# Optimization experiments

Measured on AMD Instinct MI355X. Metric: run time of the kernel, lower is better.

The kernel has to match this reference:

```python
import jax, jax.numpy as jnp
import numpy as np

EPS = 1e-5
NEG_SLOPE = 0.1  # GeoTransformer UnaryBlock uses LeakyReLU(0.1)
GROUPS = 32


def linear(x, W, b):
    # torch nn.Linear convention: W is (out, in)
    return x @ W.T + b


def group_norm(x, gamma, beta, groups=GROUPS):
    # x: (N, C). Torch applies GroupNorm on (1, C, N): stats over (C//g * N) per group.
    N, C = x.shape
    xg = x.T.reshape(groups, -1)            # (g, C//g * N)
    m = xg.mean(axis=1, keepdims=True)
    v = xg.var(axis=1, keepdims=True)
    xn = ((xg - m) / jnp.sqrt(v + EPS)).reshape(C, N).T
    return xn * gamma + beta


def unary_block(x, W, b, gamma, beta):
    return jax.nn.leaky_relu(group_norm(linear(x, W, b), gamma, beta), NEG_SLOPE)


def setup_inputs() -> dict:
    key = jax.random.key(0)
    ks = jax.random.split(key, 24)
    init_dim = 64
    N2, N3, N4, N5 = 131072, 32768, 8192, 2048
    d2, d3, d4, d5 = init_dim * 4, init_dim * 8, init_dim * 16, 2048
    out_dim = 256
    s = lambda k, shp: jax.random.normal(k, shp, dtype=jnp.float32)
    inp = {
        'feats_s2': s(ks[0], (N2, d2)),
        'feats_s3': s(ks[1], (N3, d3)),
        'feats_s4': s(ks[2], (N4, d4)),
        'feats_s5': s(ks[3], (N5, d5)),
        'up1': jax.random.randint(ks[4], (N2,), 0, N3),
        'up2': jax.random.randint(ks[5], (N3,), 0, N4),
        'up3': jax.random.randint(ks[6], (N4,), 0, N5),
        # inproj: Linear(input_dim, init_dim*32)
        'W_in': s(ks[7], (init_dim * 32, d5)) * 0.02,
        'b_in': s(ks[8], (init_dim * 32,)) * 0.02,
        # decoder4: UnaryBlock(init_dim*48, init_dim*16)
        'W4': s(ks[9], (init_dim * 16, init_dim * 48)) * 0.02,
        'b4': s(ks[10], (init_dim * 16,)) * 0.02,
        'g4': jnp.ones((init_dim * 16,), jnp.float32),
        'beta4': jnp.zeros((init_dim * 16,), jnp.float32),
        # decoder3: UnaryBlock(init_dim*24, init_dim*8)
        'W3': s(ks[11], (init_dim * 8, init_dim * 24)) * 0.02,
        'b3': s(ks[12], (init_dim * 8,)) * 0.02,
        'g3': jnp.ones((init_dim * 8,), jnp.float32),
        'beta3': jnp.zeros((init_dim * 8,), jnp.float32),
        # decoder2: LastUnaryBlock(init_dim*12, output_dim) -> plain Linear
        'W2': s(ks[13], (out_dim, init_dim * 12)) * 0.02,
        'b2': s(ks[14], (out_dim,)) * 0.02,
    }
    return inp


def reference(feats_s2, feats_s3, feats_s4, feats_s5, up1, up2, up3,
              W_in, b_in, W4, b4, g4, beta4, W3, b3, g3, beta3, W2, b2):
    x5 = linear(feats_s5, W_in, b_in)                     # (N5, 2048)
    l4 = jnp.concatenate([x5[up3], feats_s4], axis=1)     # gather + concat (N4, 3072)
    l4 = unary_block(l4, W4, b4, g4, beta4)               # (N4, 1024)
    l3 = jnp.concatenate([l4[up2], feats_s3], axis=1)     # (N3, 1536)
    l3 = unary_block(l3, W3, b3, g3, beta3)               # (N3, 512)
    l2 = jnp.concatenate([l3[up1], feats_s2], axis=1)     # (N2, 768)
    return linear(l2, W2, b2)                             # (N2, 256)
```

## Files before the change

### kernel.cpp

```cpp
#include <hip/hip_runtime.h>
#include <cstdint>
#include <cstddef>

#define DEVI __device__ __forceinline__
#define WAITVM0 asm volatile("s_waitcnt vmcnt(0)" ::: "memory")
#define WAITLGKM asm volatile("s_waitcnt lgkmcnt(0)" ::: "memory")

typedef __bf16 bf16x8 __attribute__((ext_vector_type(8)));
typedef float f32x4 __attribute__((ext_vector_type(4)));
typedef uint32_t u32x4 __attribute__((ext_vector_type(4)));

DEVI ushort f2bf(float f) {
  union { float f; uint32_t u; } v; v.f = f;
  uint32_t u = v.u;
  return (ushort)((u + 0x7FFFu + ((u >> 16) & 1u)) >> 16);
}
DEVI float bf2f(ushort h) {
  union { uint32_t u; float f; } v; v.u = ((uint32_t)h) << 16;
  return v.f;
}
DEVI float lrelu(float t) { return t > 0.0f ? t : 0.1f * t; }

DEVI u32x4 cvt8(f32x4 a, f32x4 b) {
  u32x4 o;
  o[0] = (uint32_t)f2bf(a[0]) | ((uint32_t)f2bf(a[1]) << 16);
  o[1] = (uint32_t)f2bf(a[2]) | ((uint32_t)f2bf(a[3]) << 16);
  o[2] = (uint32_t)f2bf(b[0]) | ((uint32_t)f2bf(b[1]) << 16);
  o[3] = (uint32_t)f2bf(b[2]) | ((uint32_t)f2bf(b[3]) << 16);
  return o;
}
DEVI u32x4 gn8(u32x4 d, f32x4 g0, f32x4 g1, f32x4 b0, f32x4 b1) {
  float f0 = bf2f((ushort)(d[0] & 0xffffu)), f1 = bf2f((ushort)(d[0] >> 16));
  float f2 = bf2f((ushort)(d[1] & 0xffffu)), f3 = bf2f((ushort)(d[1] >> 16));
  float f4 = bf2f((ushort)(d[2] & 0xffffu)), f5 = bf2f((ushort)(d[2] >> 16));
  float f6 = bf2f((ushort)(d[3] & 0xffffu)), f7 = bf2f((ushort)(d[3] >> 16));
  float t0 = lrelu(f0 * g0[0] + b0[0]), t1 = lrelu(f1 * g0[1] + b0[1]);
  float t2 = lrelu(f2 * g0[2] + b0[2]), t3 = lrelu(f3 * g0[3] + b0[3]);
  float t4 = lrelu(f4 * g1[0] + b1[0]), t5 = lrelu(f5 * g1[1] + b1[1]);
  float t6 = lrelu(f6 * g1[2] + b1[2]), t7 = lrelu(f7 * g1[3] + b1[3]);
  u32x4 o;
  o[0] = (uint32_t)f2bf(t0) | ((uint32_t)f2bf(t1) << 16);
  o[1] = (uint32_t)f2bf(t2) | ((uint32_t)f2bf(t3) << 16);
  o[2] = (uint32_t)f2bf(t4) | ((uint32_t)f2bf(t5) << 16);
  o[3] = (uint32_t)f2bf(t6) | ((uint32_t)f2bf(t7) << 16);
  return o;
}

DEVI void async_copy16(const void* g, void* l) {
  __attribute__((address_space(1))) void* gp =
      reinterpret_cast<__attribute__((address_space(1))) void*>(
          reinterpret_cast<uintptr_t>(const_cast<void*>(g)));
  __attribute__((address_space(3))) void* lp =
      reinterpret_cast<__attribute__((address_space(3))) void*>(
          static_cast<uint32_t>(reinterpret_cast<uintptr_t>(l)));
  __builtin_amdgcn_global_load_lds(gp, lp, 16, 0, 0);
}

struct CvtSeg { const f32x4* src; u32x4* dst; };
struct CvtArgs { CvtSeg seg[4]; int start[5]; };

__global__ void cvt_multi(CvtArgs a, int total8) {
  int i = blockIdx.x * blockDim.x + threadIdx.x;
  const int stride = gridDim.x * blockDim.x;
  for (; i < total8; i += stride) {
    int s = 0;
#pragma unroll
    for (int j = 1; j < 4; ++j) s += (i >= a.start[j]);
    const int off = i - a.start[s];
    f32x4 f0 = a.seg[s].src[off * 2];
    f32x4 f1 = a.seg[s].src[off * 2 + 1];
    a.seg[s].dst[off] = cvt8(f0, f1);
  }
}

__global__ void zero_kernel(float* __restrict__ p) { p[threadIdx.x] = 0.0f; }

__global__ void gn_coef(const float* __restrict__ stats, const float* __restrict__ gamma,
                        const float* __restrict__ beta, float* __restrict__ ga,
                        float* __restrict__ be, int C, float invcnt) {
  int ch = blockIdx.x * blockDim.x + threadIdx.x;
  if (ch >= C) return;
  int g = ch / (C >> 5);
  float mean = stats[2 * g] * invcnt;
  float var = stats[2 * g + 1] * invcnt - mean * mean;
  float inv = rsqrtf(var + 1e-5f);
  float gm = gamma[ch] * inv;
  ga[ch] = gm;
  be[ch] = beta[ch] - mean * gm;
}

__global__ void gn_apply(const ushort* __restrict__ x, const float* __restrict__ ga,
                         const float* __restrict__ be, ushort* __restrict__ y,
                         int Nrows, int C) {
  const int tpr = C >> 3;
  const int gtid = blockIdx.x * blockDim.x + threadIdx.x;
  const int c8 = (gtid % tpr) * 8;
  const f32x4 g0 = *(const f32x4*)(ga + c8), g1 = *(const f32x4*)(ga + c8 + 4);
  const f32x4 b0 = *(const f32x4*)(be + c8), b1 = *(const f32x4*)(be + c8 + 4);
  const int rstep = (gridDim.x * blockDim.x) / tpr;
  for (int r = gtid / tpr; r < Nrows; r += rstep) {
    u32x4 d = *(const u32x4*)(x + (size_t)r * C + c8);
    *(u32x4*)(y + (size_t)r * C + c8) = gn8(d, g0, g1, b0, b1);
  }
}

template <int FM, int EPI, int STATS>
__global__ __launch_bounds__(256, FM == 2 ? 3 : 2) void gemmx(
    const ushort* __restrict__ Ag, const float* __restrict__ Adf,
    const int* __restrict__ up, int dg,
    const ushort* __restrict__ Bw, const float* __restrict__ bias,
    void* __restrict__ Cout, float* __restrict__ stats,
    int M, int N, int K) {
  constexpr int BM = 32 * FM, BN = 128, BK = 64;
  constexpr int ABY = BM * BK * 2;
  constexpr int BUF = ABY + BN * BK * 2;
  __shared__ __align__(16) char smem[2 * BUF];
  __shared__ int s_up[BM];
  __shared__ float ssum[32], ssq[32];

  const int nbn = N >> 7;
  const int cpx = (int)gridDim.x >> 3;
  const int bid = ((int)blockIdx.x & 7) * cpx + ((int)blockIdx.x >> 3);
  const int bm = bid / nbn, bn = bid % nbn;
  const int row0 = bm * BM, col0 = bn * BN;
  const int tid = threadIdx.x, lane = tid & 63, wave = tid >> 6;
  const int wm = wave >> 1, wn = wave & 1;
  const int dd = K - dg;
  const int ng = dg / BK;
  const int nt = K / BK;

  if (up != nullptr && tid < BM) s_up[tid] = up[row0 + tid];
  if constexpr (STATS) { if (tid < 32) { ssum[tid] = 0.f; ssq[tid] = 0.f; } }
  __syncthreads();

  int cs_[FM];
  const ushort* pG[FM]; const float* pD[FM];
#pragma unroll
  for (int li = 0; li < FM; ++li) {
    const int chunk = li * 256 + tid;
    const int r = chunk >> 3;
    cs_[li] = ((chunk & 7) ^ (r & 7)) << 3;
    pG[li] = (ng > 0) ? (Ag + (size_t)s_up[r] * dg + cs_[li]) : nullptr;
    pD[li] = (ng < nt) ? (Adf + (size_t)(row0 + r) * dd + cs_[li]) : nullptr;
  }
  const ushort* pB[4];
#pragma unroll
  for (int li = 0; li < 4; ++li) {
    const int chunk = li * 256 + tid;
    const int rb = chunk >> 3;
    pB[li] = Bw + (size_t)(col0 + rb) * K + (((chunk & 7) ^ (rb & 7)) << 3);
  }

  f32x4 rdv[2 * FM];

  auto issueA = [&](int t, char* buf) {
    const int k0 = t * BK;
    if (t < ng) {
#pragma unroll
      for (int li = 0; li < FM; ++li)
        async_copy16(pG[li] + k0, buf + li * 4096 + wave * 1024);
    } else {
      const int kd = k0 - dg;
#pragma unroll
      for (int li = 0; li < FM; ++li) {
        rdv[2 * li]     = *(const f32x4*)(pD[li] + kd);
        rdv[2 * li + 1] = *(const f32x4*)(pD[li] + kd + 4);
      }
    }
  };
  auto consumeD = [&](char* buf) {
#pragma unroll
    for (int li = 0; li < FM; ++li)
      *(u32x4*)(buf + li * 4096 + tid * 16) = cvt8(rdv[2 * li], rdv[2 * li + 1]);
  };
  auto issueB = [&](int t, char* buf) {
#pragma unroll
    for (int li = 0; li < 4; ++li)
      async_copy16(pB[li] + t * BK, buf + ABY + li * 4096 + wave * 1024);
  };

  int offA[2][FM], offB[2][4];
#pragma unroll
  for (int kk = 0; kk < 2; ++kk) {
    const int ch = kk * 4 + (lane >> 4);
#pragma unroll
    for (int m = 0; m < FM; ++m) {
      const int ra = wm * 16 * FM + m * 16 + (lane & 15);
      offA[kk][m] = ra * 128 + ((ch ^ (ra & 7)) << 4);
    }
#pragma unroll
    for (int n = 0; n < 4; ++n) {
      const int rb = wn * 64 + n * 16 + (lane & 15);
      offB[kk][n] = ABY + rb * 128 + ((ch ^ (rb & 7)) << 4);
    }
  }

  issueA(0, smem);
  __builtin_amdgcn_sched_barrier(0);
  issueB(0, smem);
  WAITVM0;
  if (ng == 0) consumeD(smem);
  WAITLGKM;
  __builtin_amdgcn_sched_barrier(0);
  __builtin_amdgcn_s_barrier();

  f32x4 acc[FM][4] = {};
  for (int t = 0; t < nt; ++t) {
    char* cur = smem + (t & 1) * BUF;
    char* nxt = smem + ((t + 1) & 1) * BUF;
    const bool pf = (t + 1) < nt;
    if (pf) {
      issueA(t + 1, nxt);
      __builtin_amdgcn_sched_barrier(0);
      issueB(t + 1, nxt);
    }
#pragma unroll
    for (int kk = 0; kk < 2; ++kk) {
      bf16x8 af[FM], bv[4];
#pragma unroll
      for (int m = 0; m < FM; ++m) af[m] = *(const bf16x8*)(cur + offA[kk][m]);
#pragma unroll
      for (int n = 0; n < 4; ++n) bv[n] = *(const bf16x8*)(cur + offB[kk][n]);
      __builtin_amdgcn_s_setprio(1);
#pragma unroll
      for (int m = 0; m < FM; ++m)
#pragma unroll
        for (int n = 0; n < 4; ++n)
          acc[m][n] = __builtin_amdgcn_mfma_f32_16x16x32_bf16(af[m], bv[n], acc[m][n], 0, 0, 0);
      __builtin_amdgcn_s_setprio(0);
    }
    WAITVM0;
    if (pf && (t + 1) >= ng) consumeD(nxt);
    WAITLGKM;
    __builtin_amdgcn_sched_barrier(0);
    __builtin_amdgcn_s_barrier();
  }

  const int cr = (lane >> 4) << 2;
  const int cc = lane & 15;
  float sacc[4] = {0, 0, 0, 0}, qacc[4] = {0, 0, 0, 0};
#pragma unroll
  for (int n = 0; n < 4; ++n) {
    const int colg = col0 + wn * 64 + n * 16 + cc;
    const float bvv = bias[colg];
#pragma unroll
    for (int m = 0; m < FM; ++m) {
      const int rowg = row0 + wm * 16 * FM + m * 16 + cr;
#pragma unroll
      for (int r2 = 0; r2 < 4; ++r2) {
        const float v = acc[m][n][r2] + bvv;
        if constexpr (STATS) { sacc[n] += v; qacc[n] += v * v; }
        if constexpr (EPI == 0)
          ((ushort*)Cout)[(size_t)(rowg + r2) * N + colg] = f2bf(v);
        else
          ((float*)Cout)[(size_t)(rowg + r2) * N + colg] = v;
      }
    }
  }
  if constexpr (STATS) {
    const int gsize = N >> 5;
#pragma unroll
    for (int n = 0; n < 4; ++n) {
      float s = sacc[n], q = qacc[n];
      s += __shfl_xor(s, 16); q += __shfl_xor(q, 16);
      s += __shfl_xor(s, 32); q += __shfl_xor(q, 32);
      if (lane < 16) {
        const int colg = col0 + wn * 64 + n * 16 + lane;
        const int g = colg / gsize;
        atomicAdd(&ssum[g], s);
        atomicAdd(&ssq[g], q);
      }
    }
    __syncthreads();
    if (tid < 32) {
      const int g0 = col0 / gsize, g1 = (col0 + BN) / gsize;
      if (tid >= g0 && tid < g1) {
        atomicAdd(&stats[2 * tid], ssum[tid]);
        atomicAdd(&stats[2 * tid + 1], ssq[tid]);
      }
    }
  }
}

extern "C" void kernel_launch(void* const* d_in, const int* in_sizes, int n_in,
                              void* d_out, int out_size, void* d_ws, size_t ws_size,
                              hipStream_t stream) {
  const float* s2   = (const float*)d_in[0];
  const float* s3   = (const float*)d_in[1];
  const float* s4   = (const float*)d_in[2];
  const float* s5   = (const float*)d_in[3];
  const int*   up1  = (const int*)d_in[4];
  const int*   up2  = (const int*)d_in[5];
  const int*   up3  = (const int*)d_in[6];
  const float* W_in = (const float*)d_in[7];
  const float* b_in = (const float*)d_in[8];
  const float* W4   = (const float*)d_in[9];
  const float* b4   = (const float*)d_in[10];
  const float* g4   = (const float*)d_in[11];
  const float* bt4  = (const float*)d_in[12];
  const float* W3   = (const float*)d_in[13];
  const float* b3   = (const float*)d_in[14];
  const float* g3   = (const float*)d_in[15];
  const float* bt3  = (const float*)d_in[16];
  const float* W2   = (const float*)d_in[17];
  const float* b2   = (const float*)d_in[18];
  float* out = (float*)d_out;
  char* ws = (char*)d_ws;

  ushort* Winb  = (ushort*)(ws + 0);
  ushort* W4b   = (ushort*)(ws + 8388608);
  ushort* W3b   = (ushort*)(ws + 14680064);
  ushort* W2b   = (ushort*)(ws + 16252928);
  float*  stats = (float*)(ws + 16646144);
  float*  cga4  = (float*)(ws + 16646656);
  float*  cbe4  = (float*)(ws + 16650752);
  float*  cga3  = (float*)(ws + 16654848);
  float*  cbe3  = (float*)(ws + 16656896);
  ushort* x5b   = (ushort*)(ws + 16777216);
  ushort* l4lin = (ushort*)(ws + 25165824);
  ushort* l4b   = (ushort*)(ws + 41943040);
  ushort* l3lin = (ushort*)(ws + 58720256);
  ushort* l3b   = (ushort*)(ws + 92274688);

  zero_kernel<<<1, 128, 0, stream>>>(stats);

  CvtArgs ca;
  const float* srcs[4] = { W_in, W4, W3, W2 };
  ushort* dsts[4] = { Winb, W4b, W3b, W2b };
  long ns[4] = { 2048L*2048, 1024L*3072, 512L*1536, 256L*768 };
  int cum = 0;
  for (int i = 0; i < 4; ++i) {
    ca.seg[i].src = (const f32x4*)srcs[i];
    ca.seg[i].dst = (u32x4*)dsts[i];
    ca.start[i] = cum;
    cum += (int)(ns[i] >> 3);
  }
  ca.start[4] = cum;
  cvt_multi<<<1024, 256, 0, stream>>>(ca, cum);

  gemmx<2, 0, 0><<<512, 256, 0, stream>>>(
      nullptr, s5, nullptr, 0, Winb, b_in, x5b, nullptr, 2048, 2048, 2048);
  gemmx<4, 0, 1><<<512, 256, 0, stream>>>(
      x5b, s4, up3, 2048, W4b, b4, l4lin, stats, 8192, 1024, 3072);
  gn_coef<<<4, 256, 0, stream>>>(stats, g4, bt4, cga4, cbe4, 1024, 1.0f / 262144.0f);
  gn_apply<<<2048, 256, 0, stream>>>(l4lin, cga4, cbe4, l4b, 8192, 1024);
  gemmx<4, 0, 1><<<1024, 256, 0, stream>>>(
      l4b, s3, up2, 1024, W3b, b3, l3lin, stats + 64, 32768, 512, 1536);
  gn_coef<<<2, 256, 0, stream>>>(stats + 64, g3, bt3, cga3, cbe3, 512, 1.0f / 524288.0f);
  gn_apply<<<2048, 256, 0, stream>>>(l3lin, cga3, cbe3, l3b, 32768, 512);
  gemmx<4, 1, 0><<<2048, 256, 0, stream>>>(
      l3b, s2, up1, 512, W2b, b2, out, nullptr, 131072, 256, 768);

  (void)in_sizes; (void)n_in; (void)out_size; (void)ws_size;
}
```

Before: 358.7 us.

## Triple-buffer GEMM pipeline with prefetch depth two and fixed 64-row tiles

```diff
diff --git a/kernel.cpp b/kernel.cpp
--- a/kernel.cpp
+++ b/kernel.cpp
@@ -4,7 +4,11 @@
 
 #define DEVI __device__ __forceinline__
 #define WAITVM0 asm volatile("s_waitcnt vmcnt(0)" ::: "memory")
+#define WAITVM4 asm volatile("s_waitcnt vmcnt(4)" ::: "memory")
+#define WAITVM6 asm volatile("s_waitcnt vmcnt(6)" ::: "memory")
+#define WAITVM8 asm volatile("s_waitcnt vmcnt(8)" ::: "memory")
 #define WAITLGKM asm volatile("s_waitcnt lgkmcnt(0)" ::: "memory")
+#define SCHEDB __builtin_amdgcn_sched_barrier(0)
 
 typedef __bf16 bf16x8 __attribute__((ext_vector_type(8)));
 typedef float f32x4 __attribute__((ext_vector_type(4)));
@@ -104,17 +108,17 @@
   }
 }
 
-template <int FM, int EPI, int STATS>
-__global__ __launch_bounds__(256, FM == 2 ? 3 : 2) void gemmx(
+template <int EPI, int STATS>
+__global__ __launch_bounds__(256, 2) void gemmp(
     const ushort* __restrict__ Ag, const float* __restrict__ Adf,
     const int* __restrict__ up, int dg,
     const ushort* __restrict__ Bw, const float* __restrict__ bias,
     void* __restrict__ Cout, float* __restrict__ stats,
     int M, int N, int K) {
-  constexpr int BM = 32 * FM, BN = 128, BK = 64;
+  constexpr int BM = 64, BN = 128, BK = 64;
   constexpr int ABY = BM * BK * 2;
   constexpr int BUF = ABY + BN * BK * 2;
-  __shared__ __align__(16) char smem[2 * BUF];
+  __shared__ __align__(16) char smem[3 * BUF];
   __shared__ int s_up[BM];
   __shared__ float ssum[32], ssq[32];
 
@@ -133,10 +137,10 @@
   if constexpr (STATS) { if (tid < 32) { ssum[tid] = 0.f; ssq[tid] = 0.f; } }
   __syncthreads();
 
-  int cs_[FM];
-  const ushort* pG[FM]; const float* pD[FM];
-#pragma unroll
-  for (int li = 0; li < FM; ++li) {
+  int cs_[2];
+  const ushort* pG[2]; const float* pD[2];
+#pragma unroll
+  for (int li = 0; li < 2; ++li) {
     const int chunk = li * 256 + tid;
     const int r = chunk >> 3;
     cs_[li] = ((chunk & 7) ^ (r & 7)) << 3;
@@ -151,18 +155,18 @@
     pB[li] = Bw + (size_t)(col0 + rb) * K + (((chunk & 7) ^ (rb & 7)) << 3);
   }
 
-  f32x4 rdv[2 * FM];
+  f32x4 rdv[4];
 
   auto issueA = [&](int t, char* buf) {
     const int k0 = t * BK;
     if (t < ng) {
 #pragma unroll
-      for (int li = 0; li < FM; ++li)
+      for (int li = 0; li < 2; ++li)
         async_copy16(pG[li] + k0, buf + li * 4096 + wave * 1024);
     } else {
       const int kd = k0 - dg;
 #pragma unroll
-      for (int li = 0; li < FM; ++li) {
+      for (int li = 0; li < 2; ++li) {
         rdv[2 * li]     = *(const f32x4*)(pD[li] + kd);
         rdv[2 * li + 1] = *(const f32x4*)(pD[li] + kd + 4);
       }
@@ -170,7 +174,7 @@
   };
   auto consumeD = [&](char* buf) {
 #pragma unroll
-    for (int li = 0; li < FM; ++li)
+    for (int li = 0; li < 2; ++li)
       *(u32x4*)(buf + li * 4096 + tid * 16) = cvt8(rdv[2 * li], rdv[2 * li + 1]);
   };
   auto issueB = [&](int t, char* buf) {
@@ -179,13 +183,13 @@
       async_copy16(pB[li] + t * BK, buf + ABY + li * 4096 + wave * 1024);
   };
 
-  int offA[2][FM], offB[2][4];
+  int offA[2][2], offB[2][4];
 #pragma unroll
   for (int kk = 0; kk < 2; ++kk) {
     const int ch = kk * 4 + (lane >> 4);
 #pragma unroll
-    for (int m = 0; m < FM; ++m) {
-      const int ra = wm * 16 * FM + m * 16 + (lane & 15);
+    for (int m = 0; m < 2; ++m) {
+      const int ra = wm * 32 + m * 16 + (lane & 15);
       offA[kk][m] = ra * 128 + ((ch ^ (ra & 7)) << 4);
     }
 #pragma unroll
@@ -195,44 +199,59 @@
     }
   }
 
-  issueA(0, smem);
-  __builtin_amdgcn_sched_barrier(0);
-  issueB(0, smem);
-  WAITVM0;
-  if (ng == 0) consumeD(smem);
+  issueA(0, smem); issueB(0, smem);
+  if (ng == 0) { WAITVM4; SCHEDB; consumeD(smem); }
+  issueA(1, smem + BUF); issueB(1, smem + BUF);
+  if (1 < ng) { WAITVM6; } else { WAITVM8; }
   WAITLGKM;
-  __builtin_amdgcn_sched_barrier(0);
+  SCHEDB;
   __builtin_amdgcn_s_barrier();
 
-  f32x4 acc[FM][4] = {};
+  f32x4 acc[2][4] = {};
   for (int t = 0; t < nt; ++t) {
-    char* cur = smem + (t & 1) * BUF;
-    char* nxt = smem + ((t + 1) & 1) * BUF;
-    const bool pf = (t + 1) < nt;
-    if (pf) {
-      issueA(t + 1, nxt);
-      __builtin_amdgcn_sched_barrier(0);
-      issueB(t + 1, nxt);
-    }
-#pragma unroll
-    for (int kk = 0; kk < 2; ++kk) {
-      bf16x8 af[FM], bv[4];
-#pragma unroll
-      for (int m = 0; m < FM; ++m) af[m] = *(const bf16x8*)(cur + offA[kk][m]);
-#pragma unroll
-      for (int n = 0; n < 4; ++n) bv[n] = *(const bf16x8*)(cur + offB[kk][n]);
+    char* cur  = smem + (t % 3) * BUF;
+    char* nxt1 = smem + ((t + 1) % 3) * BUF;
+    char* nxt2 = smem + ((t + 2) % 3) * BUF;
+    if (t + 1 < nt && t + 1 >= ng) {
+      WAITVM4;
+      SCHEDB;
+      consumeD(nxt1);
+    }
+    {
+      bf16x8 af[2], bv[4];
+#pragma unroll
+      for (int m = 0; m < 2; ++m) af[m] = *(const bf16x8*)(cur + offA[0][m]);
+#pragma unroll
+      for (int n = 0; n < 4; ++n) bv[n] = *(const bf16x8*)(cur + offB[0][n]);
+      if (t + 2 < nt) issueA(t + 2, nxt2);
       __builtin_amdgcn_s_setprio(1);
 #pragma unroll
-      for (int m = 0; m < FM; ++m)
+      for (int m = 0; m < 2; ++m)
 #pragma unroll
         for (int n = 0; n < 4; ++n)
           acc[m][n] = __builtin_amdgcn_mfma_f32_16x16x32_bf16(af[m], bv[n], acc[m][n], 0, 0, 0);
       __builtin_amdgcn_s_setprio(0);
     }
-    WAITVM0;
-    if (pf && (t + 1) >= ng) consumeD(nxt);
+    {
+      bf16x8 af[2], bv[4];
+#pragma unroll
+      for (int m = 0; m < 2; ++m) af[m] = *(const bf16x8*)(cur + offA[1][m]);
+#pragma unroll
+      for (int n = 0; n < 4; ++n) bv[n] = *(const bf16x8*)(cur + offB[1][n]);
+      if (t + 2 < nt) issueB(t + 2, nxt2);
+      __builtin_amdgcn_s_setprio(1);
+#pragma unroll
+      for (int m = 0; m < 2; ++m)
+#pragma unroll
+        for (int n = 0; n < 4; ++n)
+          acc[m][n] = __builtin_amdgcn_mfma_f32_16x16x32_bf16(af[m], bv[n], acc[m][n], 0, 0, 0);
+      __builtin_amdgcn_s_setprio(0);
+    }
+    if (t + 2 >= nt)      { WAITVM0; }
+    else if (t + 2 < ng)  { WAITVM6; }
+    else                  { WAITVM8; }
     WAITLGKM;
-    __builtin_amdgcn_sched_barrier(0);
+    SCHEDB;
     __builtin_amdgcn_s_barrier();
   }
 
@@ -244,8 +263,8 @@
     const int colg = col0 + wn * 64 + n * 16 + cc;
     const float bvv = bias[colg];
 #pragma unroll
-    for (int m = 0; m < FM; ++m) {
-      const int rowg = row0 + wm * 16 * FM + m * 16 + cr;
+    for (int m = 0; m < 2; ++m) {
+      const int rowg = row0 + wm * 32 + m * 16 + cr;
 #pragma unroll
       for (int r2 = 0; r2 < 4; ++r2) {
         const float v = acc[m][n][r2] + bvv;
@@ -338,17 +357,17 @@
   ca.start[4] = cum;
   cvt_multi<<<1024, 256, 0, stream>>>(ca, cum);
 
-  gemmx<2, 0, 0><<<512, 256, 0, stream>>>(
+  gemmp<0, 0><<<512, 256, 0, stream>>>(
       nullptr, s5, nullptr, 0, Winb, b_in, x5b, nullptr, 2048, 2048, 2048);
-  gemmx<4, 0, 1><<<512, 256, 0, stream>>>(
+  gemmp<0, 1><<<1024, 256, 0, stream>>>(
       x5b, s4, up3, 2048, W4b, b4, l4lin, stats, 8192, 1024, 3072);
   gn_coef<<<4, 256, 0, stream>>>(stats, g4, bt4, cga4, cbe4, 1024, 1.0f / 262144.0f);
   gn_apply<<<2048, 256, 0, stream>>>(l4lin, cga4, cbe4, l4b, 8192, 1024);
-  gemmx<4, 0, 1><<<1024, 256, 0, stream>>>(
+  gemmp<0, 1><<<2048, 256, 0, stream>>>(
       l4b, s3, up2, 1024, W3b, b3, l3lin, stats + 64, 32768, 512, 1536);
   gn_coef<<<2, 256, 0, stream>>>(stats + 64, g3, bt3, cga3, cbe3, 512, 1.0f / 524288.0f);
   gn_apply<<<2048, 256, 0, stream>>>(l3lin, cga3, cbe3, l3b, 32768, 512);
-  gemmx<4, 1, 0><<<2048, 256, 0, stream>>>(
+  gemmp<1, 0><<<4096, 256, 0, stream>>>(
       l3b, s2, up1, 512, W2b, b2, out, nullptr, 131072, 256, 768);
 
   (void)in_sizes; (void)n_in; (void)out_size; (void)ws_size;
```

Result: slower. 454.7 us (+26.8%).

## Switch GEMM to single-buffered LDS with register prefetch of direct operand

Applied to the files above, without the earlier changes.

```diff
diff --git a/kernel.cpp b/kernel.cpp
--- a/kernel.cpp
+++ b/kernel.cpp
@@ -4,7 +4,10 @@
 
 #define DEVI __device__ __forceinline__
 #define WAITVM0 asm volatile("s_waitcnt vmcnt(0)" ::: "memory")
+#define WAITVM4 asm volatile("s_waitcnt vmcnt(4)" ::: "memory")
+#define WAITVM8 asm volatile("s_waitcnt vmcnt(8)" ::: "memory")
 #define WAITLGKM asm volatile("s_waitcnt lgkmcnt(0)" ::: "memory")
+#define SCHEDB __builtin_amdgcn_sched_barrier(0)
 
 typedef __bf16 bf16x8 __attribute__((ext_vector_type(8)));
 typedef float f32x4 __attribute__((ext_vector_type(4)));
@@ -104,17 +107,16 @@
   }
 }
 
-template <int FM, int EPI, int STATS>
-__global__ __launch_bounds__(256, FM == 2 ? 3 : 2) void gemmx(
+template <int EPI, int STATS>
+__global__ __launch_bounds__(256, 3) void gemms(
     const ushort* __restrict__ Ag, const float* __restrict__ Adf,
     const int* __restrict__ up, int dg,
     const ushort* __restrict__ Bw, const float* __restrict__ bias,
     void* __restrict__ Cout, float* __restrict__ stats,
     int M, int N, int K) {
-  constexpr int BM = 32 * FM, BN = 128, BK = 64;
+  constexpr int BM = 128, BN = 128, BK = 64;
   constexpr int ABY = BM * BK * 2;
-  constexpr int BUF = ABY + BN * BK * 2;
-  __shared__ __align__(16) char smem[2 * BUF];
+  __shared__ __align__(16) char smem[ABY + BN * BK * 2];
   __shared__ int s_up[BM];
   __shared__ float ssum[32], ssq[32];
 
@@ -133,10 +135,10 @@
   if constexpr (STATS) { if (tid < 32) { ssum[tid] = 0.f; ssq[tid] = 0.f; } }
   __syncthreads();
 
-  int cs_[FM];
-  const ushort* pG[FM]; const float* pD[FM];
-#pragma unroll
-  for (int li = 0; li < FM; ++li) {
+  int cs_[4];
+  const ushort* pG[4]; const float* pD[4];
+#pragma unroll
+  for (int li = 0; li < 4; ++li) {
     const int chunk = li * 256 + tid;
     const int r = chunk >> 3;
     cs_[li] = ((chunk & 7) ^ (r & 7)) << 3;
@@ -151,41 +153,39 @@
     pB[li] = Bw + (size_t)(col0 + rb) * K + (((chunk & 7) ^ (rb & 7)) << 3);
   }
 
-  f32x4 rdv[2 * FM];
-
-  auto issueA = [&](int t, char* buf) {
-    const int k0 = t * BK;
-    if (t < ng) {
-#pragma unroll
-      for (int li = 0; li < FM; ++li)
-        async_copy16(pG[li] + k0, buf + li * 4096 + wave * 1024);
-    } else {
-      const int kd = k0 - dg;
-#pragma unroll
-      for (int li = 0; li < FM; ++li) {
-        rdv[2 * li]     = *(const f32x4*)(pD[li] + kd);
-        rdv[2 * li + 1] = *(const f32x4*)(pD[li] + kd + 4);
-      }
-    }
+  f32x4 rdv[8];
+
+  auto issueAg = [&](int t) {
+#pragma unroll
+    for (int li = 0; li < 4; ++li)
+      async_copy16(pG[li] + t * BK, smem + li * 4096 + wave * 1024);
   };
-  auto consumeD = [&](char* buf) {
-#pragma unroll
-    for (int li = 0; li < FM; ++li)
-      *(u32x4*)(buf + li * 4096 + tid * 16) = cvt8(rdv[2 * li], rdv[2 * li + 1]);
+  auto issueB = [&](int t) {
+#pragma unroll
+    for (int li = 0; li < 4; ++li)
+      async_copy16(pB[li] + t * BK, smem + ABY + li * 4096 + wave * 1024);
   };
-  auto issueB = [&](int t, char* buf) {
+  auto issueRdv = [&](int t) {
+    const int kd = t * BK - dg;
+#pragma unroll
+    for (int li = 0; li < 4; ++li) {
+      rdv[2 * li]     = *(const f32x4*)(pD[li] + kd);
+      rdv[2 * li + 1] = *(const f32x4*)(pD[li] + kd + 4);
+    }
+  };
+  auto dsWrite = [&]() {
 #pragma unroll
     for (int li = 0; li < 4; ++li)
-      async_copy16(pB[li] + t * BK, buf + ABY + li * 4096 + wave * 1024);
+      *(u32x4*)(smem + li * 4096 + tid * 16) = cvt8(rdv[2 * li], rdv[2 * li + 1]);
   };
 
-  int offA[2][FM], offB[2][4];
+  int offA[2][4], offB[2][4];
 #pragma unroll
   for (int kk = 0; kk < 2; ++kk) {
     const int ch = kk * 4 + (lane >> 4);
 #pragma unroll
-    for (int m = 0; m < FM; ++m) {
-      const int ra = wm * 16 * FM + m * 16 + (lane & 15);
+    for (int m = 0; m < 4; ++m) {
+      const int ra = wm * 64 + m * 16 + (lane & 15);
       offA[kk][m] = ra * 128 + ((ch ^ (ra & 7)) << 4);
     }
 #pragma unroll
@@ -195,44 +195,39 @@
     }
   }
 
-  issueA(0, smem);
-  __builtin_amdgcn_sched_barrier(0);
-  issueB(0, smem);
-  WAITVM0;
-  if (ng == 0) consumeD(smem);
-  WAITLGKM;
-  __builtin_amdgcn_sched_barrier(0);
-  __builtin_amdgcn_s_barrier();
-
-  f32x4 acc[FM][4] = {};
+  if (ng == 0) issueRdv(0);
+
+  f32x4 acc[4][4] = {};
   for (int t = 0; t < nt; ++t) {
-    char* cur = smem + (t & 1) * BUF;
-    char* nxt = smem + ((t + 1) & 1) * BUF;
-    const bool pf = (t + 1) < nt;
-    if (pf) {
-      issueA(t + 1, nxt);
-      __builtin_amdgcn_sched_barrier(0);
-      issueB(t + 1, nxt);
-    }
+    const bool curD = (t >= ng);
+    const bool nxtDirect = (t + 1 < nt) && (t + 1 >= ng);
+    if (!curD) issueAg(t);
+    issueB(t);
+    if (curD) {
+      WAITVM4;
+      SCHEDB;
+      dsWrite();
+    }
+    if (nxtDirect) issueRdv(t + 1);
+    if (nxtDirect) { WAITVM8; } else { WAITVM0; }
+    WAITLGKM;
+    SCHEDB;
+    __builtin_amdgcn_s_barrier();
 #pragma unroll
     for (int kk = 0; kk < 2; ++kk) {
-      bf16x8 af[FM], bv[4];
-#pragma unroll
-      for (int m = 0; m < FM; ++m) af[m] = *(const bf16x8*)(cur + offA[kk][m]);
-#pragma unroll
-      for (int n = 0; n < 4; ++n) bv[n] = *(const bf16x8*)(cur + offB[kk][n]);
+      bf16x8 af[4], bv[4];
+#pragma unroll
+      for (int m = 0; m < 4; ++m) af[m] = *(const bf16x8*)(smem + offA[kk][m]);
+#pragma unroll
+      for (int n = 0; n < 4; ++n) bv[n] = *(const bf16x8*)(smem + offB[kk][n]);
       __builtin_amdgcn_s_setprio(1);
 #pragma unroll
-      for (int m = 0; m < FM; ++m)
+      for (int m = 0; m < 4; ++m)
 #pragma unroll
         for (int n = 0; n < 4; ++n)
           acc[m][n] = __builtin_amdgcn_mfma_f32_16x16x32_bf16(af[m], bv[n], acc[m][n], 0, 0, 0);
       __builtin_amdgcn_s_setprio(0);
     }
-    WAITVM0;
-    if (pf && (t + 1) >= ng) consumeD(nxt);
-    WAITLGKM;
-    __builtin_amdgcn_sched_barrier(0);
     __builtin_amdgcn_s_barrier();
   }
 
@@ -244,8 +239,8 @@
     const int colg = col0 + wn * 64 + n * 16 + cc;
     const float bvv = bias[colg];
 #pragma unroll
-    for (int m = 0; m < FM; ++m) {
-      const int rowg = row0 + wm * 16 * FM + m * 16 + cr;
+    for (int m = 0; m < 4; ++m) {
+      const int rowg = row0 + wm * 64 + m * 16 + cr;
 #pragma unroll
       for (int r2 = 0; r2 < 4; ++r2) {
         const float v = acc[m][n][r2] + bvv;
@@ -338,17 +333,17 @@
   ca.start[4] = cum;
   cvt_multi<<<1024, 256, 0, stream>>>(ca, cum);
 
-  gemmx<2, 0, 0><<<512, 256, 0, stream>>>(
+  gemms<0, 0><<<256, 256, 0, stream>>>(
       nullptr, s5, nullptr, 0, Winb, b_in, x5b, nullptr, 2048, 2048, 2048);
-  gemmx<4, 0, 1><<<512, 256, 0, stream>>>(
+  gemms<0, 1><<<512, 256, 0, stream>>>(
       x5b, s4, up3, 2048, W4b, b4, l4lin, stats, 8192, 1024, 3072);
   gn_coef<<<4, 256, 0, stream>>>(stats, g4, bt4, cga4, cbe4, 1024, 1.0f / 262144.0f);
   gn_apply<<<2048, 256, 0, stream>>>(l4lin, cga4, cbe4, l4b, 8192, 1024);
-  gemmx<4, 0, 1><<<1024, 256, 0, stream>>>(
+  gemms<0, 1><<<1024, 256, 0, stream>>>(
       l4b, s3, up2, 1024, W3b, b3, l3lin, stats + 64, 32768, 512, 1536);
   gn_coef<<<2, 256, 0, stream>>>(stats + 64, g3, bt3, cga3, cbe3, 512, 1.0f / 524288.0f);
   gn_apply<<<2048, 256, 0, stream>>>(l3lin, cga3, cbe3, l3b, 32768, 512);
-  gemmx<4, 1, 0><<<2048, 256, 0, stream>>>(
+  gemms<1, 0><<<2048, 256, 0, stream>>>(
       l3b, s2, up1, 512, W2b, b2, out, nullptr, 131072, 256, 768);
 
   (void)in_sizes; (void)n_in; (void)out_size; (void)ws_size;
```

New measurement: 323.8 us (median of 2 runs). -9.7%, faster.
